# Kernel optimization log

Measured on AMD Instinct MI355X. Metric: run time of the kernel, lower is better.

## Reference

```python
import jax, jax.numpy as jnp
import numpy as np

N = 100000          # nodes
E = 1600000         # edges (before self-loops)
F_IN = 512          # num_node_features
H1, C1 = 8, 8       # layer-1 heads, per-head channels
NUM_CLASSES = 40
NEG_SLOPE = 0.2     # PyG GATConv default


def setup_inputs() -> dict:
    key = jax.random.key(0)
    ks = jax.random.split(key, 10)
    x = jax.random.normal(ks[0], (N, F_IN), jnp.float32)
    edge_index = jax.random.randint(ks[1], (2, E), 0, N, dtype=jnp.int64)
    # Glorot-ish scaled params (matches PyG init scale qualitatively)
    W1 = jax.random.normal(ks[2], (F_IN, H1 * C1), jnp.float32) / np.sqrt(F_IN)
    a_src1 = jax.random.normal(ks[3], (H1, C1), jnp.float32) / np.sqrt(C1)
    a_dst1 = jax.random.normal(ks[4], (H1, C1), jnp.float32) / np.sqrt(C1)
    b1 = jnp.zeros((H1 * C1,), jnp.float32)
    W2 = jax.random.normal(ks[5], (H1 * C1, NUM_CLASSES), jnp.float32) / np.sqrt(H1 * C1)
    a_src2 = jax.random.normal(ks[6], (1, NUM_CLASSES), jnp.float32) / np.sqrt(NUM_CLASSES)
    a_dst2 = jax.random.normal(ks[7], (1, NUM_CLASSES), jnp.float32) / np.sqrt(NUM_CLASSES)
    b2 = jnp.zeros((NUM_CLASSES,), jnp.float32)
    return {"x": x, "edge_index": edge_index, "W1": W1, "a_src1": a_src1,
            "a_dst1": a_dst1, "b1": b1, "W2": W2, "a_src2": a_src2,
            "a_dst2": a_dst2, "b2": b2}


def gat_layer(x, src, dst, W, a_s, a_d, b, concat):
    """PyG GATConv (eval mode: dropout=0). src -> dst messages, softmax over dst."""
    heads, ch = a_s.shape
    n = x.shape[0]
    h = (x @ W).reshape(n, heads, ch)                      # [N,H,C]
    alpha_s = jnp.einsum('nhc,hc->nh', h, a_s)             # [N,H]
    alpha_d = jnp.einsum('nhc,hc->nh', h, a_d)
    e = jax.nn.leaky_relu(alpha_s[src] + alpha_d[dst], NEG_SLOPE)   # [E,H]
    # segment softmax over incoming edges of each dst node
    m = jax.ops.segment_max(e, dst, num_segments=n)        # [N,H]
    p = jnp.exp(e - m[dst])
    s = jax.ops.segment_sum(p, dst, num_segments=n)
    alpha = p / (s[dst] + 1e-16)                           # [E,H]
    out = jax.ops.segment_sum(h[src] * alpha[..., None], dst, num_segments=n)  # [N,H,C]
    out = out.reshape(n, heads * ch) if concat else out.mean(axis=1)
    return out + b


def reference(x, edge_index, W1, a_src1, a_dst1, b1, W2, a_src2, a_dst2, b2):
    n = x.shape[0]
    loops = jnp.arange(n, dtype=edge_index.dtype)
    src = jnp.concatenate([edge_index[0], loops])          # add self-loops (PyG default)
    dst = jnp.concatenate([edge_index[1], loops])
    h = gat_layer(x, src, dst, W1, a_src1, a_dst1, b1, concat=True)
    h = jax.nn.elu(h)
    out = gat_layer(h, src, dst, W2, a_src2, a_dst2, b2, concat=False)
    return jax.nn.log_softmax(out, axis=1)
```

## Files before the change

### kernel.cpp

```cpp
#include <hip/hip_runtime.h>
#include <hip/hip_bf16.h>

#define F_IN 512
#define HC1 64
#define NH1 8
#define NC 40
#define NEG_SLOPE 0.2f
#define SCAN_CHUNK 2048
#define RADIX_EPB 4096
#define MAXNB 512

typedef short bf16x8 __attribute__((ext_vector_type(8)));
typedef float f32x4 __attribute__((ext_vector_type(4)));

static __device__ __forceinline__ unsigned short f2b(float f) {
    __hip_bfloat16 h = __float2bfloat16(f);
    return *(unsigned short*)&h;
}
static __device__ __forceinline__ float b2f(unsigned short u) {
    union { unsigned int i; float f; } v;
    v.i = ((unsigned int)u) << 16;
    return v.f;
}

__global__ void detect_i64(const int* __restrict__ ei, int* __restrict__ flag, int n_check) {
    __shared__ int found;
    if (threadIdx.x == 0) found = 0;
    __syncthreads();
    for (int i = threadIdx.x; i < n_check; i += 256) {
        if (ei[2 * i + 1] != 0) atomicOr(&found, 1);
    }
    __syncthreads();
    if (threadIdx.x == 0) *flag = (found == 0) ? 1 : 0;
}

__global__ void hist_kernel(const int* __restrict__ ei, const int* __restrict__ flag,
                            int* __restrict__ deg, int E) {
    int e = blockIdx.x * 256 + threadIdx.x;
    if (e >= E) return;
    int f = *flag;
    int d = f ? ei[2 * (E + e)] : ei[E + e];
    atomicAdd(&deg[d], 1);
}

__global__ __launch_bounds__(256) void scan1(const int* __restrict__ deg, int* __restrict__ rowptr,
                                             int* __restrict__ bsums, int n) {
    __shared__ int sbuf[256];
    int tid = threadIdx.x;
    int base = blockIdx.x * SCAN_CHUNK + tid * 8;
    int v[8];
#pragma unroll
    for (int j = 0; j < 8; j++) { int idx = base + j; v[j] = (idx < n) ? deg[idx] : 0; }
    int tsum = 0;
#pragma unroll
    for (int j = 0; j < 8; j++) tsum += v[j];
    sbuf[tid] = tsum;
    __syncthreads();
    for (int off = 1; off < 256; off <<= 1) {
        int t = (tid >= off) ? sbuf[tid - off] : 0;
        __syncthreads();
        sbuf[tid] += t;
        __syncthreads();
    }
    int run = sbuf[tid] - tsum;
#pragma unroll
    for (int j = 0; j < 8; j++) {
        run += v[j];
        int idx = base + j;
        if (idx < n) rowptr[1 + idx] = run;
    }
    if (tid == 255) bsums[blockIdx.x] = sbuf[255];
}

__global__ void scan2(int* __restrict__ bsums, int nb) {
    int lane = threadIdx.x & 63;
    int v = (lane < nb) ? bsums[lane] : 0;
    int orig = v;
    for (int off = 1; off < 64; off <<= 1) {
        int t = __shfl_up(v, (unsigned)off, 64);
        if (lane >= off) v += t;
    }
    if (lane < nb) bsums[lane] = v - orig;
}

__global__ void scan3(const int* __restrict__ deg, int* __restrict__ rowptr,
                      int* __restrict__ bcur, const int* __restrict__ bsums, int n) {
    int i = blockIdx.x * 256 + threadIdx.x;
    if (i >= n) return;
    int off = bsums[i >> 11];
    int incl = rowptr[1 + i] + off;
    rowptr[1 + i] = incl;
    if ((i & 255) == 0) bcur[i >> 8] = incl - deg[i];
    if (i == 0) rowptr[0] = 0;
}

__global__ __launch_bounds__(256) void scatter1(const int* __restrict__ ei, const int* __restrict__ flag,
                                                int* __restrict__ bcur, int2* __restrict__ pairs,
                                                int E, int NB) {
    __shared__ int cnt[MAXNB];
    __shared__ int gb[MAXNB];
    int tid = threadIdx.x;
    for (int i = tid; i < NB; i += 256) cnt[i] = 0;
    __syncthreads();
    int f = *flag;
    int base = blockIdx.x * RADIX_EPB;
    int sv[16], dv[16], rv[16];
#pragma unroll
    for (int i = 0; i < 16; i++) {
        int e = base + i * 256 + tid;
        if (e < E) {
            int s, d;
            if (f) { s = ei[2 * e]; d = ei[2 * (E + e)]; }
            else   { s = ei[e];     d = ei[E + e]; }
            sv[i] = s; dv[i] = d;
            rv[i] = atomicAdd(&cnt[d >> 8], 1);
        }
    }
    __syncthreads();
    for (int i = tid; i < NB; i += 256) {
        int c = cnt[i];
        gb[i] = c ? atomicAdd(&bcur[i], c) : 0;
    }
    __syncthreads();
#pragma unroll
    for (int i = 0; i < 16; i++) {
        int e = base + i * 256 + tid;
        if (e < E) {
            int pos = gb[dv[i] >> 8] + rv[i];
            pairs[pos] = make_int2(sv[i], dv[i]);
        }
    }
}

__global__ __launch_bounds__(256) void scatter2(const int2* __restrict__ pairs,
                                                const int* __restrict__ rowptr,
                                                int* __restrict__ col, int Nn) {
    __shared__ int cur[256];
    int b = blockIdx.x;
    int node0 = b << 8;
    int tid = threadIdx.x;
    int nlast = min(node0 + 256, Nn);
    if (node0 + tid < nlast) cur[tid] = rowptr[node0 + tid];
    __syncthreads();
    int jb = rowptr[node0];
    int je = rowptr[nlast];
    for (int j = jb + tid; j < je; j += 256) {
        int2 pr = pairs[j];
        int pos = atomicAdd(&cur[pr.y - node0], 1);
        col[pos] = pr.x;
    }
}

__global__ __launch_bounds__(256) void gemm1(const float* __restrict__ x, const float* __restrict__ W,
                                             const float* __restrict__ a_s, const float* __restrict__ a_d,
                                             unsigned short* __restrict__ h1, float* __restrict__ as1,
                                             float* __restrict__ ad1, int Nn) {
    __shared__ unsigned short xs[64][72];
    __shared__ unsigned short wsT[64][72];
    int tid = threadIdx.x;
    int m0 = blockIdx.x * 64;
    int w = tid >> 6, lane = tid & 63;
    int quad = lane >> 4, mr = lane & 15;
    f32x4 acc[4];
#pragma unroll
    for (int i = 0; i < 4; i++) acc[i] = (f32x4){0.f, 0.f, 0.f, 0.f};

    int lrow = tid >> 4;
    int lf4 = tid & 15;

    for (int k0 = 0; k0 < F_IN; k0 += 64) {
        float4 xv[4], wv[4];
#pragma unroll
        for (int i = 0; i < 4; i++) {
            int row = i * 16 + lrow;
            xv[i] = (m0 + row < Nn) ? *(const float4*)(x + (size_t)(m0 + row) * F_IN + k0 + lf4 * 4)
                                    : make_float4(0.f, 0.f, 0.f, 0.f);
            wv[i] = *(const float4*)(W + (size_t)(k0 + row) * HC1 + lf4 * 4);
        }
        __syncthreads();
#pragma unroll
        for (int i = 0; i < 4; i++) {
            int row = i * 16 + lrow;
            xs[row][lf4 * 4 + 0] = f2b(xv[i].x);
            xs[row][lf4 * 4 + 1] = f2b(xv[i].y);
            xs[row][lf4 * 4 + 2] = f2b(xv[i].z);
            xs[row][lf4 * 4 + 3] = f2b(xv[i].w);
            wsT[lf4 * 4 + 0][row] = f2b(wv[i].x);
            wsT[lf4 * 4 + 1][row] = f2b(wv[i].y);
            wsT[lf4 * 4 + 2][row] = f2b(wv[i].z);
            wsT[lf4 * 4 + 3][row] = f2b(wv[i].w);
        }
        __syncthreads();
#pragma unroll
        for (int ks = 0; ks < 2; ks++) {
            bf16x8 a = *(const bf16x8*)&xs[w * 16 + mr][ks * 32 + quad * 8];
#pragma unroll
            for (int nb = 0; nb < 4; nb++) {
                bf16x8 b = *(const bf16x8*)&wsT[nb * 16 + mr][ks * 32 + quad * 8];
                acc[nb] = __builtin_amdgcn_mfma_f32_16x16x32_bf16(a, b, acc[nb], 0, 0, 0);
            }
        }
    }
    __syncthreads();
    unsigned short (*hs)[72] = xs;
#pragma unroll
    for (int nb = 0; nb < 4; nb++)
#pragma unroll
        for (int r = 0; r < 4; r++)
            hs[w * 16 + quad * 4 + r][nb * 16 + mr] = f2b(acc[nb][r]);
    __syncthreads();
    {
        int srow = tid >> 2, sseg = tid & 3;
        if (m0 + srow < Nn) {
            uint4 v0 = *(const uint4*)&hs[srow][sseg * 16];
            uint4 v1 = *(const uint4*)&hs[srow][sseg * 16 + 8];
            uint4* dst = (uint4*)(h1 + (size_t)(m0 + srow) * HC1 + sseg * 16);
            dst[0] = v0;
            dst[1] = v1;
        }
    }
    for (int i = tid; i < 512; i += 256) {
        int row = i >> 3, hh = i & 7;
        if (m0 + row < Nn) {
            float s = 0.f, d = 0.f;
#pragma unroll
            for (int c = 0; c < 8; c++) {
                float v = b2f(hs[row][hh * 8 + c]);
                s += v * a_s[hh * 8 + c];
                d += v * a_d[hh * 8 + c];
            }
            as1[(size_t)(m0 + row) * NH1 + hh] = s;
            ad1[(size_t)(m0 + row) * NH1 + hh] = d;
        }
    }
}

__device__ __forceinline__ float lrelu(float e) { return e > 0.f ? e : NEG_SLOPE * e; }

__global__ __launch_bounds__(256) void agg1(const unsigned short* __restrict__ h1,
                                            const float* __restrict__ as1,
                                            const float* __restrict__ ad1, const int* __restrict__ rowptr,
                                            const int* __restrict__ col, const float* __restrict__ b1,
                                            float* __restrict__ h2, int Nn) {
    __shared__ float pbuf[4][NH1 * 68];
    int w = threadIdx.x >> 6;
    int wave = (blockIdx.x * 256 + threadIdx.x) >> 6;
    int lane = threadIdx.x & 63;
    if (wave >= Nn) return;
    int d = wave;
    int jb = rowptr[d], je = rowptr[d + 1];
    const float4* as4 = (const float4*)as1;
    const float4* ad4 = (const float4*)ad1;

    float4 sd0 = as4[d * 2], sd1 = as4[d * 2 + 1];
    float4 dd0 = ad4[d * 2], dd1 = ad4[d * 2 + 1];
    float ad[8] = {dd0.x, dd0.y, dd0.z, dd0.w, dd1.x, dd1.y, dd1.z, dd1.w};
    float sv[8] = {sd0.x, sd0.y, sd0.z, sd0.w, sd1.x, sd1.y, sd1.z, sd1.w};
    float e0[8];
#pragma unroll
    for (int h = 0; h < NH1; h++) e0[h] = lrelu(sv[h] + ad[h]);

    int myh = lane >> 3;
    float acc = b2f(h1[(size_t)d * HC1 + lane]);
    float ssum = 1.0f;
    float* pb = pbuf[w];

    for (int c0 = jb; c0 < je; c0 += 64) {
        int nc = min(64, je - c0);
        int srcv = d;
        if (lane < nc) srcv = col[c0 + lane];
        float4 a0 = as4[srcv * 2], a1 = as4[srcv * 2 + 1];
        float ev[8] = {a0.x, a0.y, a0.z, a0.w, a1.x, a1.y, a1.z, a1.w};
#pragma unroll
        for (int h = 0; h < NH1; h++)
            pb[h * 68 + lane] = __expf(lrelu(ev[h] + ad[h]) - e0[h]);

        int jj = 0;
        for (; jj + 3 < nc; jj += 4) {
            int s0 = __shfl(srcv, jj, 64), s1 = __shfl(srcv, jj + 1, 64);
            int s2 = __shfl(srcv, jj + 2, 64), s3 = __shfl(srcv, jj + 3, 64);
            float p0 = pb[myh * 68 + jj],     p1 = pb[myh * 68 + jj + 1];
            float p2 = pb[myh * 68 + jj + 2], p3 = pb[myh * 68 + jj + 3];
            float g0 = b2f(h1[(size_t)s0 * HC1 + lane]);
            float g1 = b2f(h1[(size_t)s1 * HC1 + lane]);
            float g2 = b2f(h1[(size_t)s2 * HC1 + lane]);
            float g3 = b2f(h1[(size_t)s3 * HC1 + lane]);
            ssum += (p0 + p1) + (p2 + p3);
            acc += p0 * g0 + p1 * g1 + p2 * g2 + p3 * g3;
        }
        for (; jj < nc; jj++) {
            int s0 = __shfl(srcv, jj, 64);
            float p0 = pb[myh * 68 + jj];
            ssum += p0;
            acc += p0 * b2f(h1[(size_t)s0 * HC1 + lane]);
        }
    }
    float o = acc / (ssum + 1e-16f) + b1[lane];
    o = o > 0.f ? o : __expf(o) - 1.0f;
    h2[(size_t)d * HC1 + lane] = o;
}

__global__ __launch_bounds__(256) void gemm2(const float* __restrict__ h2, const float* __restrict__ W2,
                                             const float* __restrict__ av_in, const float* __restrict__ dv_in,
                                             float* __restrict__ g, float* __restrict__ as2,
                                             float* __restrict__ ad2, int Nn) {
    __shared__ float W2s[HC1 * NC];
    __shared__ float hrow[4][HC1];
    __shared__ float avec[NC], dvec[NC];
    int tid = threadIdx.x;
    for (int i = tid; i < HC1 * NC; i += 256) W2s[i] = W2[i];
    if (tid < NC) { avec[tid] = av_in[tid]; dvec[tid] = dv_in[tid]; }
    int w = tid >> 6, lane = tid & 63;
    int n = blockIdx.x * 4 + w;
    float hv = 0.f;
    if (n < Nn) hv = h2[(size_t)n * HC1 + lane];
    hrow[w][lane] = hv;
    __syncthreads();
    float acc = 0.f;
    bool act = (n < Nn) && (lane < NC);
    if (act) {
#pragma unroll
        for (int k = 0; k < HC1; k++) acc += hrow[w][k] * W2s[k * NC + lane];
        g[(size_t)n * NC + lane] = acc;
    }
    float va = act ? acc * avec[lane] : 0.f;
    float vd = act ? acc * dvec[lane] : 0.f;
    for (int off = 32; off; off >>= 1) {
        va += __shfl_xor(va, off, 64);
        vd += __shfl_xor(vd, off, 64);
    }
    if (n < Nn && lane == 0) { as2[n] = va; ad2[n] = vd; }
}

__global__ __launch_bounds__(256) void agg2(const float* __restrict__ g, const float* __restrict__ as2,
                                            const float* __restrict__ ad2, const int* __restrict__ rowptr,
                                            const int* __restrict__ col, const float* __restrict__ b2,
                                            float* __restrict__ out, int Nn) {
    __shared__ float pbuf[4][64];
    int w = threadIdx.x >> 6;
    int wave = (blockIdx.x * 256 + threadIdx.x) >> 6;
    int lane = threadIdx.x & 63;
    if (wave >= Nn) return;
    int d = wave;
    int jb = rowptr[d], je = rowptr[d + 1];
    float adv = ad2[d];
    float e0 = lrelu(as2[d] + adv);
    float acc = (lane < NC) ? g[(size_t)d * NC + lane] : 0.f;
    float ssum = 1.0f;
    float* pb = pbuf[w];

    for (int c0 = jb; c0 < je; c0 += 64) {
        int nc = min(64, je - c0);
        int srcv = d;
        if (lane < nc) srcv = col[c0 + lane];
        pb[lane] = __expf(lrelu(as2[srcv] + adv) - e0);

        int jj = 0;
        for (; jj + 3 < nc; jj += 4) {
            int s0 = __shfl(srcv, jj, 64), s1 = __shfl(srcv, jj + 1, 64);
            int s2 = __shfl(srcv, jj + 2, 64), s3 = __shfl(srcv, jj + 3, 64);
            float p0 = pb[jj], p1 = pb[jj + 1], p2 = pb[jj + 2], p3 = pb[jj + 3];
            float g0 = 0.f, g1 = 0.f, g2 = 0.f, g3 = 0.f;
            if (lane < NC) {
                g0 = g[(size_t)s0 * NC + lane];
                g1 = g[(size_t)s1 * NC + lane];
                g2 = g[(size_t)s2 * NC + lane];
                g3 = g[(size_t)s3 * NC + lane];
            }
            ssum += (p0 + p1) + (p2 + p3);
            acc += p0 * g0 + p1 * g1 + p2 * g2 + p3 * g3;
        }
        for (; jj < nc; jj++) {
            int s0 = __shfl(srcv, jj, 64);
            float p0 = pb[jj];
            ssum += p0;
            if (lane < NC) acc += p0 * g[(size_t)s0 * NC + lane];
        }
    }
    float o = acc / (ssum + 1e-16f) + ((lane < NC) ? b2[lane] : 0.f);
    float vm = (lane < NC) ? o : -1e30f;
#pragma unroll
    for (int off = 32; off; off >>= 1) vm = fmaxf(vm, __shfl_xor(vm, off, 64));
    float ex = (lane < NC) ? __expf(o - vm) : 0.f;
#pragma unroll
    for (int off = 32; off; off >>= 1) ex += __shfl_xor(ex, off, 64);
    float lsm = o - vm - __logf(ex);
    if (lane < NC) out[(size_t)d * NC + lane] = lsm;
}

extern "C" void kernel_launch(void* const* d_in, const int* in_sizes, int n_in,
                              void* d_out, int out_size, void* d_ws, size_t ws_size,
                              hipStream_t stream) {
    const float* x      = (const float*)d_in[0];
    const int*   ei     = (const int*)d_in[1];
    const float* W1     = (const float*)d_in[2];
    const float* a_src1 = (const float*)d_in[3];
    const float* a_dst1 = (const float*)d_in[4];
    const float* b1     = (const float*)d_in[5];
    const float* W2     = (const float*)d_in[6];
    const float* a_src2 = (const float*)d_in[7];
    const float* a_dst2 = (const float*)d_in[8];
    const float* b2     = (const float*)d_in[9];
    float* out = (float*)d_out;

    const int N = in_sizes[0] / F_IN;
    const int E = in_sizes[1] / 2;
    const int NB = (N + 255) >> 8;

    char* p = (char*)d_ws;
    auto alloc = [&](size_t bytes) -> void* {
        void* r = (void*)p;
        p += (bytes + 255) & ~(size_t)255;
        return r;
    };
    int2* pairs = (int2*)alloc((size_t)E * 8);
    int* deg    = (int*)alloc((size_t)N * 4);
    int* rowptr = (int*)alloc(((size_t)N + 1) * 4);
    int* bcur   = (int*)alloc((size_t)MAXNB * 4);
    int* bsums  = (int*)alloc(64 * 4);
    int* flag   = (int*)alloc(256);
    int* col    = (int*)alloc((size_t)E * 4);
    unsigned short* h1 = (unsigned short*)alloc((size_t)N * HC1 * 4);
    float* as1  = (float*)alloc((size_t)N * NH1 * 4);
    float* ad1  = (float*)alloc((size_t)N * NH1 * 4);
    float* h2   = (float*)alloc((size_t)N * HC1 * 4);
    float* g    = (float*)h1;
    float* as2  = as1;
    float* ad2  = ad1;

    hipMemsetAsync(deg, 0, (size_t)N * 4, stream);
    detect_i64<<<1, 256, 0, stream>>>(ei, flag, 4096);
    int ge = (E + 255) / 256;
    hist_kernel<<<ge, 256, 0, stream>>>(ei, flag, deg, E);
    int nb = (N + SCAN_CHUNK - 1) / SCAN_CHUNK;
    scan1<<<nb, 256, 0, stream>>>(deg, rowptr, bsums, N);
    scan2<<<1, 64, 0, stream>>>(bsums, nb);
    scan3<<<(N + 255) / 256, 256, 0, stream>>>(deg, rowptr, bcur, bsums, N);
    scatter1<<<(E + RADIX_EPB - 1) / RADIX_EPB, 256, 0, stream>>>(ei, flag, bcur, pairs, E, NB);
    scatter2<<<NB, 256, 0, stream>>>(pairs, rowptr, col, N);

    gemm1<<<(N + 63) / 64, 256, 0, stream>>>(x, W1, a_src1, a_dst1, h1, as1, ad1, N);
    agg1<<<(N + 3) / 4, 256, 0, stream>>>(h1, as1, ad1, rowptr, col, b1, h2, N);

    gemm2<<<(N + 3) / 4, 256, 0, stream>>>(h2, W2, a_src2, a_dst2, g, as2, ad2, N);
    agg2<<<(N + 3) / 4, 256, 0, stream>>>(g, as2, ad2, rowptr, col, b2, out, N);
}
```

Measured before the change: 640.0 us.

## Reassociate layer-2 projection after aggregation and pre-swizzle W1 for gemm1

Removes the separate gemm2 kernel. Layer-2 attention logits are computed in agg1 by folding W2 into the attention vectors (W2·a). agg2 then aggregates the 64-wide fp16 hidden features and applies W2 once per node after normalization. A prep kernel pre-converts W1 to bf16 in a swizzled layout so gemm1 loads it with vector copies and reads LDS without bank conflicts. This drops one full-N kernel and the intermediate fp32 h2/g round trips. In exchange, agg2 gathers 64 fp16 values per edge instead of 40 fp32, and every block reloads W2 into LDS.

```diff
diff --git a/kernel.cpp b/kernel.cpp
--- a/kernel.cpp
+++ b/kernel.cpp
@@ -1,5 +1,6 @@
 #include <hip/hip_runtime.h>
 #include <hip/hip_bf16.h>
+#include <hip/hip_fp16.h>
 
 #define F_IN 512
 #define HC1 64
@@ -22,6 +23,14 @@
     v.i = ((unsigned int)u) << 16;
     return v.f;
 }
+static __device__ __forceinline__ unsigned short f2h(float f) {
+    __half h = __float2half(f);
+    return *(unsigned short*)&h;
+}
+static __device__ __forceinline__ float h2f(unsigned short u) {
+    __half h = *(__half*)&u;
+    return __half2float(h);
+}
 
 __global__ void detect_i64(const int* __restrict__ ei, int* __restrict__ flag, int n_check) {
     __shared__ int found;
@@ -41,6 +50,36 @@
     int f = *flag;
     int d = f ? ei[2 * (E + e)] : ei[E + e];
     atomicAdd(&deg[d], 1);
+}
+
+__global__ void prep(const float* __restrict__ W1, const float* __restrict__ W2,
+                     const float* __restrict__ a_s2, const float* __restrict__ a_d2,
+                     unsigned short* __restrict__ wst, float* __restrict__ ws2,
+                     float* __restrict__ wd2) {
+    int t = blockIdx.x * 256 + threadIdx.x;
+    if (t < 4096) {
+        int p  = t & 7;
+        int n  = (t >> 3) & 63;
+        int kb = t >> 9;
+        int l  = p ^ (n & 7);
+        int k0 = kb * 64 + l * 8;
+        unsigned short v[8];
+#pragma unroll
+        for (int j = 0; j < 8; j++) v[j] = f2b(W1[(size_t)(k0 + j) * HC1 + n]);
+        *(uint4*)(wst + ((size_t)(kb * 64 + n) * 64 + p * 8)) = *(uint4*)v;
+    }
+    if (blockIdx.x == 0 && threadIdx.x < HC1) {
+        int c = threadIdx.x;
+        float s = 0.f, d = 0.f;
+#pragma unroll
+        for (int j = 0; j < NC; j++) {
+            float w = W2[c * NC + j];
+            s += w * a_s2[j];
+            d += w * a_d2[j];
+        }
+        ws2[c] = s;
+        wd2[c] = d;
+    }
 }
 
 __global__ __launch_bounds__(256) void scan1(const int* __restrict__ deg, int* __restrict__ rowptr,
@@ -151,12 +190,14 @@
     }
 }
 
-__global__ __launch_bounds__(256) void gemm1(const float* __restrict__ x, const float* __restrict__ W,
+__global__ __launch_bounds__(256) void gemm1(const float* __restrict__ x,
+                                             const unsigned short* __restrict__ wst,
                                              const float* __restrict__ a_s, const float* __restrict__ a_d,
                                              unsigned short* __restrict__ h1, float* __restrict__ as1,
                                              float* __restrict__ ad1, int Nn) {
-    __shared__ unsigned short xs[64][72];
-    __shared__ unsigned short wsT[64][72];
+    __shared__ __align__(16) unsigned short smem[8192];
+    unsigned short* xs = smem;
+    unsigned short* ws = smem + 4096;
     int tid = threadIdx.x;
     int m0 = blockIdx.x * 64;
     int w = tid >> 6, lane = tid & 63;
@@ -165,44 +206,52 @@
 #pragma unroll
     for (int i = 0; i < 4; i++) acc[i] = (f32x4){0.f, 0.f, 0.f, 0.f};
 
-    int lrow = tid >> 4;
-    int lf4 = tid & 15;
-
-    for (int k0 = 0; k0 < F_IN; k0 += 64) {
-        float4 xv[4], wv[4];
-#pragma unroll
-        for (int i = 0; i < 4; i++) {
-            int row = i * 16 + lrow;
-            xv[i] = (m0 + row < Nn) ? *(const float4*)(x + (size_t)(m0 + row) * F_IN + k0 + lf4 * 4)
-                                    : make_float4(0.f, 0.f, 0.f, 0.f);
-            wv[i] = *(const float4*)(W + (size_t)(k0 + row) * HC1 + lf4 * 4);
-        }
+    int srow = tid >> 2;
+    int sseg = tid & 3;
+    bool rok = (m0 + srow) < Nn;
+    const float* xrow = x + (size_t)(m0 + srow) * F_IN + sseg * 16;
+    int swzw = (srow & 7) << 4;
+    int swzr = (mr & 7) << 4;
+
+    for (int kb = 0; kb < 8; kb++) {
+        float4 xv0, xv1, xv2, xv3;
+        if (rok) {
+            const float4* xp = (const float4*)(xrow + kb * 64);
+            xv0 = xp[0]; xv1 = xp[1]; xv2 = xp[2]; xv3 = xp[3];
+        } else {
+            xv0 = xv1 = xv2 = xv3 = make_float4(0.f, 0.f, 0.f, 0.f);
+        }
+        const uint4* wp = (const uint4*)(wst + (size_t)kb * 4096);
+        uint4 wv0 = wp[tid];
+        uint4 wv1 = wp[tid + 256];
         __syncthreads();
-#pragma unroll
-        for (int i = 0; i < 4; i++) {
-            int row = i * 16 + lrow;
-            xs[row][lf4 * 4 + 0] = f2b(xv[i].x);
-            xs[row][lf4 * 4 + 1] = f2b(xv[i].y);
-            xs[row][lf4 * 4 + 2] = f2b(xv[i].z);
-            xs[row][lf4 * 4 + 3] = f2b(xv[i].w);
-            wsT[lf4 * 4 + 0][row] = f2b(wv[i].x);
-            wsT[lf4 * 4 + 1][row] = f2b(wv[i].y);
-            wsT[lf4 * 4 + 2][row] = f2b(wv[i].z);
-            wsT[lf4 * 4 + 3][row] = f2b(wv[i].w);
+        {
+            unsigned short bx[16];
+            bx[0]  = f2b(xv0.x); bx[1]  = f2b(xv0.y); bx[2]  = f2b(xv0.z); bx[3]  = f2b(xv0.w);
+            bx[4]  = f2b(xv1.x); bx[5]  = f2b(xv1.y); bx[6]  = f2b(xv1.z); bx[7]  = f2b(xv1.w);
+            bx[8]  = f2b(xv2.x); bx[9]  = f2b(xv2.y); bx[10] = f2b(xv2.z); bx[11] = f2b(xv2.w);
+            bx[12] = f2b(xv3.x); bx[13] = f2b(xv3.y); bx[14] = f2b(xv3.z); bx[15] = f2b(xv3.w);
+            unsigned short* xr = xs + srow * 64;
+            *(uint4*)(xr + ((((sseg * 32)      ) ^ swzw) >> 1)) = *(uint4*)&bx[0];
+            *(uint4*)(xr + ((((sseg * 32) + 16 ) ^ swzw) >> 1)) = *(uint4*)&bx[8];
+            ((uint4*)ws)[tid]       = wv0;
+            ((uint4*)ws)[tid + 256] = wv1;
         }
         __syncthreads();
 #pragma unroll
         for (int ks = 0; ks < 2; ks++) {
-            bf16x8 a = *(const bf16x8*)&xs[w * 16 + mr][ks * 32 + quad * 8];
+            int kc = ks * 64 + quad * 16;
+            int co = (kc ^ swzr) >> 1;
+            bf16x8 a = *(const bf16x8*)(xs + (w * 16 + mr) * 64 + co);
 #pragma unroll
             for (int nb = 0; nb < 4; nb++) {
-                bf16x8 b = *(const bf16x8*)&wsT[nb * 16 + mr][ks * 32 + quad * 8];
+                bf16x8 b = *(const bf16x8*)(ws + (nb * 16 + mr) * 64 + co);
                 acc[nb] = __builtin_amdgcn_mfma_f32_16x16x32_bf16(a, b, acc[nb], 0, 0, 0);
             }
         }
     }
     __syncthreads();
-    unsigned short (*hs)[72] = xs;
+    unsigned short (*hs)[72] = (unsigned short(*)[72])smem;
 #pragma unroll
     for (int nb = 0; nb < 4; nb++)
 #pragma unroll
@@ -210,8 +259,7 @@
             hs[w * 16 + quad * 4 + r][nb * 16 + mr] = f2b(acc[nb][r]);
     __syncthreads();
     {
-        int srow = tid >> 2, sseg = tid & 3;
-        if (m0 + srow < Nn) {
+        if (rok) {
             uint4 v0 = *(const uint4*)&hs[srow][sseg * 16];
             uint4 v1 = *(const uint4*)&hs[srow][sseg * 16 + 8];
             uint4* dst = (uint4*)(h1 + (size_t)(m0 + srow) * HC1 + sseg * 16);
@@ -241,7 +289,9 @@
                                             const float* __restrict__ as1,
                                             const float* __restrict__ ad1, const int* __restrict__ rowptr,
                                             const int* __restrict__ col, const float* __restrict__ b1,
-                                            float* __restrict__ h2, int Nn) {
+                                            const float* __restrict__ ws2, const float* __restrict__ wd2,
+                                            unsigned short* __restrict__ h2b, float* __restrict__ as2,
+                                            float* __restrict__ ad2, int Nn) {
     __shared__ float pbuf[4][NH1 * 68];
     int w = threadIdx.x >> 6;
     int wave = (blockIdx.x * 256 + threadIdx.x) >> 6;
@@ -249,6 +299,7 @@
     if (wave >= Nn) return;
     int d = wave;
     int jb = rowptr[d], je = rowptr[d + 1];
+    float w2l = ws2[lane], wd2l = wd2[lane];
     const float4* as4 = (const float4*)as1;
     const float4* ad4 = (const float4*)ad1;
 
@@ -297,55 +348,38 @@
     }
     float o = acc / (ssum + 1e-16f) + b1[lane];
     o = o > 0.f ? o : __expf(o) - 1.0f;
-    h2[(size_t)d * HC1 + lane] = o;
-}
-
-__global__ __launch_bounds__(256) void gemm2(const float* __restrict__ h2, const float* __restrict__ W2,
-                                             const float* __restrict__ av_in, const float* __restrict__ dv_in,
-                                             float* __restrict__ g, float* __restrict__ as2,
-                                             float* __restrict__ ad2, int Nn) {
-    __shared__ float W2s[HC1 * NC];
-    __shared__ float hrow[4][HC1];
-    __shared__ float avec[NC], dvec[NC];
-    int tid = threadIdx.x;
-    for (int i = tid; i < HC1 * NC; i += 256) W2s[i] = W2[i];
-    if (tid < NC) { avec[tid] = av_in[tid]; dvec[tid] = dv_in[tid]; }
-    int w = tid >> 6, lane = tid & 63;
-    int n = blockIdx.x * 4 + w;
-    float hv = 0.f;
-    if (n < Nn) hv = h2[(size_t)n * HC1 + lane];
-    hrow[w][lane] = hv;
-    __syncthreads();
-    float acc = 0.f;
-    bool act = (n < Nn) && (lane < NC);
-    if (act) {
-#pragma unroll
-        for (int k = 0; k < HC1; k++) acc += hrow[w][k] * W2s[k * NC + lane];
-        g[(size_t)n * NC + lane] = acc;
-    }
-    float va = act ? acc * avec[lane] : 0.f;
-    float vd = act ? acc * dvec[lane] : 0.f;
+    h2b[(size_t)d * HC1 + lane] = f2h(o);
+    float va = o * w2l;
+    float vd = o * wd2l;
+#pragma unroll
     for (int off = 32; off; off >>= 1) {
         va += __shfl_xor(va, off, 64);
         vd += __shfl_xor(vd, off, 64);
     }
-    if (n < Nn && lane == 0) { as2[n] = va; ad2[n] = vd; }
-}
-
-__global__ __launch_bounds__(256) void agg2(const float* __restrict__ g, const float* __restrict__ as2,
+    if (lane == 0) { as2[d] = va; ad2[d] = vd; }
+}
+
+__global__ __launch_bounds__(256) void agg2(const unsigned short* __restrict__ h2b,
+                                            const float* __restrict__ as2,
                                             const float* __restrict__ ad2, const int* __restrict__ rowptr,
-                                            const int* __restrict__ col, const float* __restrict__ b2,
+                                            const int* __restrict__ col, const float* __restrict__ W2,
+                                            const float* __restrict__ b2,
                                             float* __restrict__ out, int Nn) {
     __shared__ float pbuf[4][64];
-    int w = threadIdx.x >> 6;
-    int wave = (blockIdx.x * 256 + threadIdx.x) >> 6;
-    int lane = threadIdx.x & 63;
+    __shared__ float smv[4][64];
+    __shared__ float W2s[HC1 * NC];
+    int tid = threadIdx.x;
+    for (int i = tid; i < HC1 * NC; i += 256) W2s[i] = W2[i];
+    __syncthreads();
+    int w = tid >> 6;
+    int wave = (blockIdx.x * 256 + tid) >> 6;
+    int lane = tid & 63;
     if (wave >= Nn) return;
     int d = wave;
     int jb = rowptr[d], je = rowptr[d + 1];
     float adv = ad2[d];
     float e0 = lrelu(as2[d] + adv);
-    float acc = (lane < NC) ? g[(size_t)d * NC + lane] : 0.f;
+    float acc = h2f(h2b[(size_t)d * HC1 + lane]);
     float ssum = 1.0f;
     float* pb = pbuf[w];
 
@@ -360,13 +394,10 @@
             int s0 = __shfl(srcv, jj, 64), s1 = __shfl(srcv, jj + 1, 64);
             int s2 = __shfl(srcv, jj + 2, 64), s3 = __shfl(srcv, jj + 3, 64);
             float p0 = pb[jj], p1 = pb[jj + 1], p2 = pb[jj + 2], p3 = pb[jj + 3];
-            float g0 = 0.f, g1 = 0.f, g2 = 0.f, g3 = 0.f;
-            if (lane < NC) {
-                g0 = g[(size_t)s0 * NC + lane];
-                g1 = g[(size_t)s1 * NC + lane];
-                g2 = g[(size_t)s2 * NC + lane];
-                g3 = g[(size_t)s3 * NC + lane];
-            }
+            float g0 = h2f(h2b[(size_t)s0 * HC1 + lane]);
+            float g1 = h2f(h2b[(size_t)s1 * HC1 + lane]);
+            float g2 = h2f(h2b[(size_t)s2 * HC1 + lane]);
+            float g3 = h2f(h2b[(size_t)s3 * HC1 + lane]);
             ssum += (p0 + p1) + (p2 + p3);
             acc += p0 * g0 + p1 * g1 + p2 * g2 + p3 * g3;
         }
@@ -374,10 +405,18 @@
             int s0 = __shfl(srcv, jj, 64);
             float p0 = pb[jj];
             ssum += p0;
-            if (lane < NC) acc += p0 * g[(size_t)s0 * NC + lane];
-        }
-    }
-    float o = acc / (ssum + 1e-16f) + ((lane < NC) ? b2[lane] : 0.f);
+            acc += p0 * h2f(h2b[(size_t)s0 * HC1 + lane]);
+        }
+    }
+    float an = acc / (ssum + 1e-16f);
+    smv[w][lane] = an;
+    float o = 0.f;
+    if (lane < NC) {
+        o = b2[lane];
+        const float* sv = smv[w];
+#pragma unroll
+        for (int c = 0; c < HC1; c++) o += sv[c] * W2s[c * NC + lane];
+    }
     float vm = (lane < NC) ? o : -1e30f;
 #pragma unroll
     for (int off = 32; off; off >>= 1) vm = fmaxf(vm, __shfl_xor(vm, off, 64));
@@ -420,16 +459,19 @@
     int* bsums  = (int*)alloc(64 * 4);
     int* flag   = (int*)alloc(256);
     int* col    = (int*)alloc((size_t)E * 4);
-    unsigned short* h1 = (unsigned short*)alloc((size_t)N * HC1 * 4);
+    unsigned short* h1  = (unsigned short*)alloc((size_t)N * HC1 * 2);
     float* as1  = (float*)alloc((size_t)N * NH1 * 4);
     float* ad1  = (float*)alloc((size_t)N * NH1 * 4);
-    float* h2   = (float*)alloc((size_t)N * HC1 * 4);
-    float* g    = (float*)h1;
-    float* as2  = as1;
-    float* ad2  = ad1;
+    unsigned short* h2b = (unsigned short*)alloc((size_t)N * HC1 * 2);
+    float* as2  = (float*)alloc((size_t)N * 4);
+    float* ad2  = (float*)alloc((size_t)N * 4);
+    unsigned short* wst = (unsigned short*)alloc(8 * 64 * 64 * 2);
+    float* ws2  = (float*)alloc(HC1 * 4);
+    float* wd2  = (float*)alloc(HC1 * 4);
 
     hipMemsetAsync(deg, 0, (size_t)N * 4, stream);
     detect_i64<<<1, 256, 0, stream>>>(ei, flag, 4096);
+    prep<<<16, 256, 0, stream>>>(W1, W2, a_src2, a_dst2, wst, ws2, wd2);
     int ge = (E + 255) / 256;
     hist_kernel<<<ge, 256, 0, stream>>>(ei, flag, deg, E);
     int nb = (N + SCAN_CHUNK - 1) / SCAN_CHUNK;
@@ -439,9 +481,8 @@
     scatter1<<<(E + RADIX_EPB - 1) / RADIX_EPB, 256, 0, stream>>>(ei, flag, bcur, pairs, E, NB);
     scatter2<<<NB, 256, 0, stream>>>(pairs, rowptr, col, N);
 
-    gemm1<<<(N + 63) / 64, 256, 0, stream>>>(x, W1, a_src1, a_dst1, h1, as1, ad1, N);
-    agg1<<<(N + 3) / 4, 256, 0, stream>>>(h1, as1, ad1, rowptr, col, b1, h2, N);
-
-    gemm2<<<(N + 3) / 4, 256, 0, stream>>>(h2, W2, a_src2, a_dst2, g, as2, ad2, N);
-    agg2<<<(N + 3) / 4, 256, 0, stream>>>(g, as2, ad2, rowptr, col, b2, out, N);
-}
+    gemm1<<<(N + 63) / 64, 256, 0, stream>>>(x, wst, a_src1, a_dst1, h1, as1, ad1, N);
+    agg1<<<(N + 3) / 4, 256, 0, stream>>>(h1, as1, ad1, rowptr, col, b1, ws2, wd2, h2b, as2, ad2, N);
+
+    agg2<<<(N + 3) / 4, 256, 0, stream>>>(h2b, as2, ad2, rowptr, col, W2, b2, out, N);
+}
```

Measured after the change: 622.3 us. 1.03x faster.
